# Kernel tuning notes

Hardware: AMD Instinct MI355X
Metric: run time of the kernel (lower is better)

Reference implementation:

```python
import jax, jax.numpy as jnp
import numpy as np

N = 50000      # nodes
E = 800000     # edges
R = 8          # relation types
IN = 128       # in_dim
OUT = 128      # out_dim
H = 8          # num_heads
HD = OUT // H  # head dim = 16


def setup_inputs() -> dict:
    key = jax.random.key(0)
    ks = jax.random.split(key, 6)
    return {
        "h": jax.random.normal(ks[0], (N, IN), dtype=jnp.float32),
        "fc_weight": jax.random.normal(ks[1], (R, IN, OUT), dtype=jnp.float32) * 0.05,
        "attn_weight": jax.random.normal(ks[2], (R, H, 2 * HD), dtype=jnp.float32) * 0.05,
        "src": jax.random.randint(ks[3], (E,), 0, N, dtype=jnp.int32),
        "dst": jax.random.randint(ks[4], (E,), 0, N, dtype=jnp.int32),
        "etype": jax.random.randint(ks[5], (E,), 0, R, dtype=jnp.int32),
    }


def reference(h, fc_weight, attn_weight, src, dst, etype):
    # Per-relation projection of ALL node features (equivalent math to the
    # per-edge gathered bmm in the original, without materializing E x IN x OUT):
    # [R, N, OUT] -> [R, N, H, HD]
    z_nodes = jnp.einsum('ni,rio->rno', h, fc_weight).reshape(R, N, H, HD)
    z_s = z_nodes[etype, src]   # [E, H, HD]  (== bmm(h[src], fc_weight[etype]))
    z_d = z_nodes[etype, dst]   # [E, H, HD]
    aw = attn_weight[etype]     # [E, H, 2*HD]
    # a = sum(cat([z_s, z_d], -1) * attn_weight[etype], -1)
    a = jnp.sum(z_s * aw[:, :, :HD], axis=2) + jnp.sum(z_d * aw[:, :, HD:], axis=2)  # [E, H]
    e = jax.nn.leaky_relu(a)    # torch F.leaky_relu_ default slope 0.01

    # Edge softmax per destination node (per head), numerically stable.
    m = jax.ops.segment_max(e, dst, num_segments=N)          # [N, H]
    m = jnp.where(jnp.isfinite(m), m, jnp.zeros_like(m))     # guard empty nodes
    ex = jnp.exp(e - m[dst])                                 # [E, H]
    denom = jax.ops.segment_sum(ex, dst, num_segments=N)     # [N, H]
    num = jax.ops.segment_sum(ex[:, :, None] * z_s, dst, num_segments=N)  # [N, H, HD]
    out = num / jnp.maximum(denom, 1e-9)[:, :, None]         # [N, H, HD]
    return out
```

## Files before the change

kernel.cpp:

```cpp
#include <hip/hip_runtime.h>

#define NN 50000
#define NE 800000
#define NR 8
#define DIN 128
#define DOUT 128
#define NH 8

#define NB_SCAN ((NN + 255) / 256)

typedef __attribute__((ext_vector_type(8))) short bf16x8;
typedef __attribute__((ext_vector_type(4))) float f32x4;

__device__ __forceinline__ unsigned short f2bf(float f) {
  unsigned u = __float_as_uint(f);
  unsigned r = (u + 0x7FFFu + ((u >> 16) & 1u)) >> 16;
  return (unsigned short)r;
}
__device__ __forceinline__ float bf2f(unsigned short b) {
  return __uint_as_float(((unsigned)b) << 16);
}

__global__ __launch_bounds__(256) void prep_hb(const float* __restrict__ h,
                                               unsigned short* __restrict__ hb) {
  int i = blockIdx.x * 256 + threadIdx.x;
  if (i >= NN * DIN / 8) return;
  const float4* p = (const float4*)(h + (size_t)i * 8);
  float4 v0 = p[0], v1 = p[1];
  ushort4 w0, w1;
  w0.x = f2bf(v0.x); w0.y = f2bf(v0.y); w0.z = f2bf(v0.z); w0.w = f2bf(v0.w);
  w1.x = f2bf(v1.x); w1.y = f2bf(v1.y); w1.z = f2bf(v1.z); w1.w = f2bf(v1.w);
  ushort4* o = (ushort4*)(hb + (size_t)i * 8);
  o[0] = w0; o[1] = w1;
}

__global__ __launch_bounds__(256) void prep_fcf(
    const float* __restrict__ fc, const float* __restrict__ attn,
    unsigned short* __restrict__ fcf) {
  int idx = blockIdx.x * 256 + threadIdx.x;
  if (idx >= NR * DIN * 144) return;
  int r = idx / (DIN * 144);
  int rem = idx - r * (DIN * 144);
  int k = rem / 144;
  int j = rem - k * 144;
  float v;
  if (j < DOUT) {
    v = fc[((size_t)r * DIN + k) * DOUT + j];
  } else {
    int cc = j - DOUT;
    int hh = cc & 7, p = cc >> 3;
    const float* fr = fc + ((size_t)r * DIN + k) * DOUT + hh * 16;
    const float* ar = attn + ((size_t)r * NH + hh) * 32 + p * 16;
    v = 0.f;
#pragma unroll
    for (int d = 0; d < 16; ++d) v += fr[d] * ar[d];
  }
  int t = j >> 4, c = j & 15, ks = k >> 5, gg = (k >> 3) & 3, i = k & 7;
  fcf[((((size_t)r * 9 + t) * 4 + ks) * 4 + gg) * 128 + c * 8 + i] = f2bf(v);
}

__global__ __launch_bounds__(256) void gemm_mfma(
    const unsigned short* __restrict__ hb, const unsigned short* __restrict__ fcf,
    unsigned short* __restrict__ z, float* __restrict__ s_buf) {
  const int r = blockIdx.y;
  const int n0 = blockIdx.x * 64;
  const int w = threadIdx.x >> 6;
  const int lane = threadIdx.x & 63;
  const int g = lane >> 4, c = lane & 15;
  const int nbase = n0 + w * 16;

  bf16x8 bf[9][4];
  const unsigned short* fb = fcf + ((size_t)r * 36 * 64 + lane) * 8;
#pragma unroll
  for (int t = 0; t < 9; ++t)
#pragma unroll
    for (int ks = 0; ks < 4; ++ks)
      bf[t][ks] = *(const bf16x8*)(fb + (size_t)(t * 4 + ks) * 512);

  int arow = nbase + c;
  if (arow > NN - 1) arow = NN - 1;
  const unsigned short* ha = hb + (size_t)arow * DIN + g * 8;
  bf16x8 af[4];
#pragma unroll
  for (int ks = 0; ks < 4; ++ks) af[ks] = *(const bf16x8*)(ha + ks * 32);

  f32x4 acc[9];
#pragma unroll
  for (int t = 0; t < 9; ++t) acc[t] = (f32x4){0.f, 0.f, 0.f, 0.f};

#pragma unroll
  for (int ks = 0; ks < 4; ++ks)
#pragma unroll
    for (int t = 0; t < 9; ++t)
      acc[t] = __builtin_amdgcn_mfma_f32_16x16x32_bf16(af[ks], bf[t][ks], acc[t], 0, 0, 0);

#pragma unroll
  for (int q = 0; q < 4; ++q) {
    int node = nbase + g * 4 + q;
    if (node < NN) {
      unsigned short* zr = z + ((size_t)r * NN + node) * DOUT + c;
#pragma unroll
      for (int t = 0; t < 8; ++t) zr[t * 16] = f2bf(acc[t][q]);
      s_buf[((size_t)r * NN + node) * 16 + c] = acc[8][q];
    }
  }
}

__global__ __launch_bounds__(256) void hist_kernel(const int* __restrict__ dst,
                                                   int* __restrict__ deg) {
  int e = blockIdx.x * blockDim.x + threadIdx.x;
  if (e < NE) atomicAdd(&deg[dst[e]], 1);
}

__global__ __launch_bounds__(256) void scan1(const int* __restrict__ deg,
                                             int* __restrict__ bsum) {
  __shared__ int ws_[4];
  int gi = blockIdx.x * 256 + threadIdx.x;
  int v = (gi < NN) ? deg[gi] : 0;
#pragma unroll
  for (int m = 1; m < 64; m <<= 1) v += __shfl_xor(v, m);
  if ((threadIdx.x & 63) == 0) ws_[threadIdx.x >> 6] = v;
  __syncthreads();
  if (threadIdx.x == 0) bsum[blockIdx.x] = ws_[0] + ws_[1] + ws_[2] + ws_[3];
}

__global__ __launch_bounds__(256) void scan2(const int* __restrict__ bsum,
                                             int* __restrict__ bbase,
                                             int* __restrict__ row_start) {
  __shared__ int part[256];
  int t = threadIdx.x;
  part[t] = (t < NB_SCAN) ? bsum[t] : 0;
  __syncthreads();
  for (int off = 1; off < 256; off <<= 1) {
    int v = (t >= off) ? part[t - off] : 0;
    __syncthreads();
    part[t] += v;
    __syncthreads();
  }
  if (t < NB_SCAN) bbase[t] = (t == 0) ? 0 : part[t - 1];
  if (t == 0) row_start[NN] = NE;
}

__global__ __launch_bounds__(256) void scan3(const int* __restrict__ deg,
                                             const int* __restrict__ bbase,
                                             int* __restrict__ row_start) {
  __shared__ int part[256];
  int t = threadIdx.x;
  int gi = blockIdx.x * 256 + t;
  int v = (gi < NN) ? deg[gi] : 0;
  part[t] = v;
  __syncthreads();
  for (int off = 1; off < 256; off <<= 1) {
    int x = (t >= off) ? part[t - off] : 0;
    __syncthreads();
    part[t] += x;
    __syncthreads();
  }
  if (gi < NN) row_start[gi] = bbase[blockIdx.x] + part[t] - v;
}

__global__ __launch_bounds__(256) void scatter_kernel(
    const int* __restrict__ src, const int* __restrict__ dst,
    const int* __restrict__ et, const float* __restrict__ s_buf,
    const int* __restrict__ row_start, int* __restrict__ cursor,
    unsigned short* __restrict__ es, unsigned* __restrict__ sidx) {
  int e = blockIdx.x * blockDim.x + threadIdx.x;
  if (e >= NE) return;
  int s = src[e], d = dst[e], r = et[e];
  int pos = row_start[d] + atomicAdd(&cursor[d], 1);
  const float4* sp = (const float4*)&s_buf[((size_t)r * NN + s) * 16];
  const float4* dp = (const float4*)&s_buf[((size_t)r * NN + d) * 16 + 8];
  float4 a0 = sp[0], a1 = sp[1], b0 = dp[0], b1 = dp[1];
  float ev[8] = {a0.x + b0.x, a0.y + b0.y, a0.z + b0.z, a0.w + b0.w,
                 a1.x + b1.x, a1.y + b1.y, a1.z + b1.z, a1.w + b1.w};
  ushort4 w0, w1;
  unsigned short wv[8];
#pragma unroll
  for (int hh = 0; hh < 8; ++hh) {
    float x = ev[hh];
    x = x > 0.f ? x : 0.01f * x;
    wv[hh] = f2bf(x);
  }
  w0.x = wv[0]; w0.y = wv[1]; w0.z = wv[2]; w0.w = wv[3];
  w1.x = wv[4]; w1.y = wv[5]; w1.z = wv[6]; w1.w = wv[7];
  *(ushort4*)&es[(size_t)pos * 8] = w0;
  *(ushort4*)&es[(size_t)pos * 8 + 4] = w1;
  sidx[pos] = (unsigned)s | ((unsigned)r << 16);
}

__global__ __launch_bounds__(256) void node_accum(
    const int* __restrict__ row_start, const unsigned short* __restrict__ es,
    const unsigned* __restrict__ sidx, const unsigned short* __restrict__ z,
    float* __restrict__ out) {
  int wave = threadIdx.x >> 6;
  int lane = threadIdx.x & 63;
  int n = blockIdx.x * 4 + wave;
  if (n >= NN) return;
  int b0 = row_start[n];
  int deg = row_start[n + 1] - b0;

  int hl = lane & 7;
  int jg = lane >> 3;
  int ho = lane >> 3;

  float maxv = -INFINITY;
  for (int j = jg; j < deg; j += 8)
    maxv = fmaxf(maxv, bf2f(es[(size_t)(b0 + j) * 8 + hl]));
#pragma unroll
  for (int m = 8; m < 64; m <<= 1) maxv = fmaxf(maxv, __shfl_xor(maxv, m));

  float2 acc = make_float2(0.f, 0.f);
  float den = 0.f;

  for (int cch = 0; cch < deg; cch += 8) {
    int j = cch + jg;
    float ex = 0.f;
    if (j < deg) ex = __expf(bf2f(es[(size_t)(b0 + j) * 8 + hl]) - maxv);
    den += ex;
    int rem = min(8, deg - cch);
    unsigned pk = sidx[b0 + cch + min(lane & 7, rem - 1)];
#pragma unroll
    for (int jj = 0; jj < 8; ++jj) {
      if (jj >= rem) break;
      float exb = __shfl(ex, (jj << 3) | ho);
      unsigned p = __shfl(pk, jj);
      unsigned sr_ = p & 0xFFFFu;
      unsigned rr = p >> 16;
      unsigned u = *(const unsigned*)&z[(((size_t)rr * NN + sr_) << 7) + 2 * lane];
      acc.x += exb * __uint_as_float((u & 0xFFFFu) << 16);
      acc.y += exb * __uint_as_float(u & 0xFFFF0000u);
    }
  }
#pragma unroll
  for (int m = 8; m < 64; m <<= 1) den += __shfl_xor(den, m);
  float deno = __shfl(den, ho);
  float inv = 1.0f / fmaxf(deno, 1e-9f);
  *(float2*)&out[((size_t)n << 7) + 2 * lane] =
      make_float2(acc.x * inv, acc.y * inv);
}

extern "C" void kernel_launch(void* const* d_in, const int* in_sizes, int n_in,
                              void* d_out, int out_size, void* d_ws, size_t ws_size,
                              hipStream_t stream) {
  const float* h = (const float*)d_in[0];
  const float* fc = (const float*)d_in[1];
  const float* attn = (const float*)d_in[2];
  const int* src = (const int*)d_in[3];
  const int* dst = (const int*)d_in[4];
  const int* et = (const int*)d_in[5];
  float* out = (float*)d_out;

  char* wsb = (char*)d_ws;
  size_t off = 0;
  unsigned short* z = (unsigned short*)(wsb + off);  off += (size_t)NR * NN * DOUT * 2;
  unsigned short* hb = (unsigned short*)(wsb + off); off += (size_t)NN * DIN * 2;
  float* s_buf = (float*)(wsb + off);                off += (size_t)NR * NN * 16 * 4;
  unsigned short* es = (unsigned short*)(wsb + off); off += (size_t)NE * NH * 2;
  unsigned* sidx = (unsigned*)(wsb + off);           off += (size_t)NE * 4;
  unsigned short* fcf = (unsigned short*)(wsb + off);off += (size_t)NR * 9 * 4 * 4 * 128 * 2;
  int* deg = (int*)(wsb + off);                      off += (size_t)NN * 4;
  int* row_start = (int*)(wsb + off);                off += (size_t)(NN + 1) * 4;
  int* cursor = (int*)(wsb + off);                   off += (size_t)NN * 4;
  int* bsum = (int*)(wsb + off);                     off += (size_t)NB_SCAN * 4;
  int* bbase = (int*)(wsb + off);                    off += (size_t)NB_SCAN * 4;

  hipMemsetAsync(deg, 0, (size_t)NN * sizeof(int), stream);
  hipMemsetAsync(cursor, 0, (size_t)NN * sizeof(int), stream);

  prep_hb<<<(NN * DIN / 8 + 255) / 256, 256, 0, stream>>>(h, hb);
  prep_fcf<<<(NR * DIN * 144 + 255) / 256, 256, 0, stream>>>(fc, attn, fcf);

  dim3 ggrid((NN + 63) / 64, NR);
  gemm_mfma<<<ggrid, 256, 0, stream>>>(hb, fcf, z, s_buf);

  hist_kernel<<<(NE + 255) / 256, 256, 0, stream>>>(dst, deg);
  scan1<<<NB_SCAN, 256, 0, stream>>>(deg, bsum);
  scan2<<<1, 256, 0, stream>>>(bsum, bbase, row_start);
  scan3<<<NB_SCAN, 256, 0, stream>>>(deg, bbase, row_start);

  scatter_kernel<<<(NE + 255) / 256, 256, 0, stream>>>(src, dst, et, s_buf,
                                                       row_start, cursor, es, sidx);

  node_accum<<<(NN + 3) / 4, 256, 0, stream>>>(row_start, es, sidx, z, out);
}
```

Baseline: 327.3 us.

## Vectorize z stores via transposed MFMA and gather 4 edges per wave step

The projection kernel swaps the MFMA operands so each lane holds 4 consecutive outputs of one node, which allows ushort4 and float4 stores instead of scattered 2-byte stores. The aggregation kernel now has each 16-lane group load a whole 256-byte z row with 16-byte loads and process 4 edges at once. Partial sums are then combined across groups with xor shuffles. This cuts the number of gather instructions and serial loop iterations per edge chunk, at the cost of more registers and an extra cross-lane reduction.

```diff
diff --git a/kernel.cpp b/kernel.cpp
--- a/kernel.cpp
+++ b/kernel.cpp
@@ -92,17 +92,20 @@
   for (int ks = 0; ks < 4; ++ks)
 #pragma unroll
     for (int t = 0; t < 9; ++t)
-      acc[t] = __builtin_amdgcn_mfma_f32_16x16x32_bf16(af[ks], bf[t][ks], acc[t], 0, 0, 0);
-
-#pragma unroll
-  for (int q = 0; q < 4; ++q) {
-    int node = nbase + g * 4 + q;
-    if (node < NN) {
-      unsigned short* zr = z + ((size_t)r * NN + node) * DOUT + c;
-#pragma unroll
-      for (int t = 0; t < 8; ++t) zr[t * 16] = f2bf(acc[t][q]);
-      s_buf[((size_t)r * NN + node) * 16 + c] = acc[8][q];
+      acc[t] = __builtin_amdgcn_mfma_f32_16x16x32_bf16(bf[t][ks], af[ks], acc[t], 0, 0, 0);
+
+  int node = nbase + c;
+  if (node < NN) {
+    unsigned short* zr = z + ((size_t)r * NN + node) * DOUT + g * 4;
+#pragma unroll
+    for (int t = 0; t < 8; ++t) {
+      ushort4 wv;
+      wv.x = f2bf(acc[t][0]); wv.y = f2bf(acc[t][1]);
+      wv.z = f2bf(acc[t][2]); wv.w = f2bf(acc[t][3]);
+      *(ushort4*)(zr + t * 16) = wv;
     }
+    float* sb = s_buf + ((size_t)r * NN + node) * 16 + g * 4;
+    *(float4*)sb = make_float4(acc[8][0], acc[8][1], acc[8][2], acc[8][3]);
   }
 }
 
@@ -201,7 +204,8 @@
 
   int hl = lane & 7;
   int jg = lane >> 3;
-  int ho = lane >> 3;
+  int c16 = lane & 15;
+  int e4 = lane >> 4;
 
   float maxv = -INFINITY;
   for (int j = jg; j < deg; j += 8)
@@ -209,8 +213,9 @@
 #pragma unroll
   for (int m = 8; m < 64; m <<= 1) maxv = fmaxf(maxv, __shfl_xor(maxv, m));
 
-  float2 acc = make_float2(0.f, 0.f);
+  float acc[8] = {0.f, 0.f, 0.f, 0.f, 0.f, 0.f, 0.f, 0.f};
   float den = 0.f;
+  int hh16 = c16 >> 1;
 
   for (int cch = 0; cch < deg; cch += 8) {
     int j = cch + jg;
@@ -220,23 +225,33 @@
     int rem = min(8, deg - cch);
     unsigned pk = sidx[b0 + cch + min(lane & 7, rem - 1)];
 #pragma unroll
-    for (int jj = 0; jj < 8; ++jj) {
-      if (jj >= rem) break;
-      float exb = __shfl(ex, (jj << 3) | ho);
-      unsigned p = __shfl(pk, jj);
+    for (int half = 0; half < 2; ++half) {
+      if (half * 4 >= rem) break;
+      int o = half * 4 + e4;
+      float exb = __shfl(ex, (o << 3) | hh16);
+      unsigned p = __shfl(pk, o);
       unsigned sr_ = p & 0xFFFFu;
       unsigned rr = p >> 16;
-      unsigned u = *(const unsigned*)&z[(((size_t)rr * NN + sr_) << 7) + 2 * lane];
-      acc.x += exb * __uint_as_float((u & 0xFFFFu) << 16);
-      acc.y += exb * __uint_as_float(u & 0xFFFF0000u);
+      bf16x8 v = *(const bf16x8*)&z[(((size_t)rr * NN + sr_) << 7) + c16 * 8];
+#pragma unroll
+      for (int i = 0; i < 8; ++i)
+        acc[i] += exb * bf2f((unsigned short)v[i]);
     }
   }
 #pragma unroll
   for (int m = 8; m < 64; m <<= 1) den += __shfl_xor(den, m);
-  float deno = __shfl(den, ho);
+#pragma unroll
+  for (int i = 0; i < 8; ++i) {
+    acc[i] += __shfl_xor(acc[i], 16);
+    acc[i] += __shfl_xor(acc[i], 32);
+  }
+  float deno = __shfl(den, hh16);
   float inv = 1.0f / fmaxf(deno, 1e-9f);
-  *(float2*)&out[((size_t)n << 7) + 2 * lane] =
-      make_float2(acc.x * inv, acc.y * inv);
+  if (lane < 16) {
+    float* ob = out + ((size_t)n << 7) + lane * 8;
+    *(float4*)ob = make_float4(acc[0] * inv, acc[1] * inv, acc[2] * inv, acc[3] * inv);
+    *(float4*)(ob + 4) = make_float4(acc[4] * inv, acc[5] * inv, acc[6] * inv, acc[7] * inv);
+  }
 }
 
 extern "C" void kernel_launch(void* const* d_in, const int* in_sizes, int n_in,
```

Result: faster. 311.8 us (-4.7%).
